# Kernel tuning notes

Measured on AMD Instinct MI355X. Metric: run time of the kernel, lower is better.

The kernel has to match this reference:

```python
import math
import jax, jax.numpy as jnp
import numpy as np

B, L, D = 2, 2048, 1024
NH = 16
HS = D // NH
BLOCK_SIZE = 2048


def setup_inputs() -> dict:
    key = jax.random.key(0)
    ks = jax.random.split(key, 4)
    x = jax.random.normal(ks[0], (B, L, D), dtype=jnp.float32)
    Wqkv = jax.random.normal(ks[1], (D, 3 * D), dtype=jnp.float32) * 0.02
    bqkv = jnp.zeros((3 * D,), dtype=jnp.float32)
    Wproj = jax.random.normal(ks[2], (D, D), dtype=jnp.float32) * 0.02
    bproj = jnp.zeros((D,), dtype=jnp.float32)
    Er = jax.random.normal(ks[3], (BLOCK_SIZE, HS), dtype=jnp.float32)
    return {"x": x, "Wqkv": Wqkv, "bqkv": bqkv, "Wproj": Wproj, "bproj": bproj, "Er": Er}


def _skew(QEr):
    # QEr: [B, nh, L, L]  (Music Transformer skew trick)
    b, nh, nr, nc = QEr.shape
    padded = jnp.pad(QEr, ((0, 0), (0, 0), (0, 0), (1, 0)))  # [B, nh, nr, nc+1]
    reshaped = padded.reshape(b, nh, nc + 1, nr)
    return reshaped[:, :, 1:, :]  # [B, nh, nr, nc]


def reference(x, Wqkv, bqkv, Wproj, bproj, Er):
    b, l, d = x.shape
    qkv = x @ Wqkv + bqkv  # [B, L, 3D]
    q, k, v = jnp.split(qkv, 3, axis=2)
    q = q.reshape(b, l, NH, HS).transpose(0, 2, 1, 3)  # [B, nh, L, hs]
    k = k.reshape(b, l, NH, HS).transpose(0, 2, 1, 3)
    v = v.reshape(b, l, NH, HS).transpose(0, 2, 1, 3)

    start = BLOCK_SIZE - l
    Er_t = Er[start:, :].T  # [hs, L]
    QEr = jnp.einsum('bhld,dm->bhlm', q, Er_t)  # [B, nh, L, L]
    Srel = _skew(QEr)

    QK_t = jnp.einsum('bhld,bhmd->bhlm', q, k)
    scale = 1.0 / math.sqrt(HS)
    att = (QK_t + Srel) * scale
    causal = jnp.tril(jnp.ones((l, l), dtype=bool))
    att = jnp.where(causal[None, None, :, :], att, jnp.float32(-jnp.inf))
    att = jax.nn.softmax(att, axis=-1)
    y = jnp.einsum('bhlm,bhmd->bhld', att, v)
    y = y.transpose(0, 2, 1, 3).reshape(b, l, d)
    return y @ Wproj + bproj
```

## Files before the change

### kernel.cpp

```cpp
#include <hip/hip_runtime.h>
#include <stdint.h>

#define BB 2
#define LL 2048
#define DD 1024
#define NHH 16
#define HSS 64

typedef __bf16 bf16x8 __attribute__((ext_vector_type(8)));
typedef float f32x4 __attribute__((ext_vector_type(4)));

__device__ __forceinline__ bf16x8 load8(const float* p) {
  float4 f0 = *(const float4*)p;
  float4 f1 = *(const float4*)(p + 4);
  bf16x8 v;
  v[0] = (__bf16)f0.x; v[1] = (__bf16)f0.y; v[2] = (__bf16)f0.z; v[3] = (__bf16)f0.w;
  v[4] = (__bf16)f1.x; v[5] = (__bf16)f1.y; v[6] = (__bf16)f1.z; v[7] = (__bf16)f1.w;
  return v;
}
__device__ __forceinline__ bf16x8 load8(const __bf16* p) {
  return *(const bf16x8*)p;
}

__device__ __forceinline__ void async_ld16(__bf16* lds_uniform_base,
                                           const __bf16* gptr_per_lane) {
  __builtin_amdgcn_global_load_lds(
      (const __attribute__((address_space(1))) void*)gptr_per_lane,
      (__attribute__((address_space(3))) void*)lds_uniform_base, 16, 0, 0);
}

__global__ void prep_k(const float* __restrict__ Wqkv, const float* __restrict__ x,
                       const float* __restrict__ Er, __bf16* __restrict__ WqkvT,
                       __bf16* __restrict__ xb, __bf16* __restrict__ Erb) {
  int tx = threadIdx.x, ty = threadIdx.y;
  int tid = ty * 32 + tx;
  if (blockIdx.z == 1) {
    if (blockIdx.x >= 2048) return;
    size_t off = ((size_t)blockIdx.x * 256 + tid) * 8;
    *(bf16x8*)&xb[off] = load8(&x[off]);
    return;
  }
  if (blockIdx.z == 2) {
    if (blockIdx.x >= 64) return;
    size_t off = ((size_t)blockIdx.x * 256 + tid) * 8;
    *(bf16x8*)&Erb[off] = load8(&Er[off]);
    return;
  }
  __shared__ __bf16 tile[32][33];
  int c0 = (blockIdx.x % 96) * 32, r0 = (blockIdx.x / 96) * 32;
#pragma unroll
  for (int i = ty; i < 32; i += 8)
    tile[i][tx] = (__bf16)Wqkv[(size_t)(r0 + i) * 3072 + c0 + tx];
  __syncthreads();
#pragma unroll
  for (int i = ty; i < 32; i += 8)
    WqkvT[(size_t)(c0 + i) * 1024 + r0 + tx] = tile[tx][i];
}

__global__ void tconv_k(const float* __restrict__ src, __bf16* __restrict__ dst,
                        int R, int C) {
  __shared__ __bf16 tile[32][33];
  int c0 = blockIdx.x * 32, r0 = blockIdx.y * 32;
  int tx = threadIdx.x, ty = threadIdx.y;
#pragma unroll
  for (int i = ty; i < 32; i += 8)
    tile[i][tx] = (__bf16)src[(size_t)(r0 + i) * C + c0 + tx];
  __syncthreads();
#pragma unroll
  for (int i = ty; i < 32; i += 8)
    dst[(size_t)(c0 + i) * R + r0 + tx] = tile[tx][i];
}

__global__ __launch_bounds__(256) void gemm_qkv_k(
    const __bf16* __restrict__ A, const __bf16* __restrict__ Bt,
    const float* __restrict__ bias, __bf16* __restrict__ Qo,
    __bf16* __restrict__ Ko, __bf16* __restrict__ Vto) {
  const int K = 1024;
  __shared__ __align__(16) __bf16 As[128 * 32];
  __shared__ __align__(16) __bf16 Bs[128 * 32];
  int t = threadIdx.x;
  int wave = t >> 6, lane = t & 63, qd = lane >> 4, lr = lane & 15;
  int m0 = blockIdx.y * 128, n0 = blockIdx.x * 128;
  int wm = (wave >> 1) * 64, wn = (wave & 1) * 64;
  f32x4 acc[4][4] = {};
  int srow = lane >> 2, sch = (lane & 3) * 8;
  const __bf16* Ab[2];
  const __bf16* Bb[2];
#pragma unroll
  for (int c = 0; c < 2; c++) {
    Ab[c] = A + (size_t)(m0 + (wave * 2 + c) * 16 + srow) * K + sch;
    Bb[c] = Bt + (size_t)(n0 + (wave * 2 + c) * 16 + srow) * K + sch;
  }
  for (int k0 = 0; k0 < K; k0 += 32) {
    __syncthreads();
#pragma unroll
    for (int c = 0; c < 2; c++) {
      async_ld16(&As[(wave * 2 + c) * 512], Ab[c] + k0);
      async_ld16(&Bs[(wave * 2 + c) * 512], Bb[c] + k0);
    }
    __syncthreads();
    bf16x8 af[4], bfr[4];
#pragma unroll
    for (int mt = 0; mt < 4; mt++)
      af[mt] = *(const bf16x8*)&As[(wm + mt * 16 + lr) * 32 + qd * 8];
#pragma unroll
    for (int nt = 0; nt < 4; nt++)
      bfr[nt] = *(const bf16x8*)&Bs[(wn + nt * 16 + lr) * 32 + qd * 8];
#pragma unroll
    for (int mt = 0; mt < 4; mt++)
#pragma unroll
      for (int nt = 0; nt < 4; nt++)
        acc[mt][nt] = __builtin_amdgcn_mfma_f32_16x16x32_bf16(af[mt], bfr[nt],
                                                              acc[mt][nt], 0, 0, 0);
  }
  float bvv[4];
#pragma unroll
  for (int nt = 0; nt < 4; nt++) bvv[nt] = bias[n0 + wn + nt * 16 + lr];
#pragma unroll
  for (int mt = 0; mt < 4; mt++)
#pragma unroll
    for (int nt = 0; nt < 4; nt++)
#pragma unroll
      for (int r = 0; r < 4; r++) {
        int row = m0 + wm + mt * 16 + qd * 4 + r;
        int col = n0 + wn + nt * 16 + lr;
        __bf16 bb = (__bf16)(acc[mt][nt][r] + bvv[nt]);
        int b = row >> 11, l = row & 2047;
        int h = (col >> 6) & 15, d = col & 63;
        if (col < DD) {
          Qo[(((size_t)(b * NHH + h)) * LL + l) * HSS + d] = bb;
        } else if (col < 2 * DD) {
          Ko[(((size_t)(b * NHH + h)) * LL + l) * HSS + d] = bb;
        } else {
          Vto[(((size_t)(b * NHH + h)) * HSS + d) * LL + l] = bb;
        }
      }
}

__global__ __launch_bounds__(256) void gemm_proj_k(
    const __bf16* __restrict__ A, const __bf16* __restrict__ Bt,
    const float* __restrict__ bias, float* __restrict__ out) {
  const int K = 1024, N = 1024;
  __shared__ __align__(16) __bf16 As[128 * 32];
  __shared__ __align__(16) __bf16 Bs[64 * 32];
  int t = threadIdx.x;
  int wave = t >> 6, lane = t & 63, qd = lane >> 4, lr = lane & 15;
  int m0 = blockIdx.y * 128, n0 = blockIdx.x * 64;
  int wm = (wave >> 1) * 64, wn = (wave & 1) * 32;
  f32x4 acc[4][2] = {};
  int srow = lane >> 2, sch = (lane & 3) * 8;
  const __bf16* Ab[2];
  const __bf16* Bb;
#pragma unroll
  for (int c = 0; c < 2; c++)
    Ab[c] = A + (size_t)(m0 + (wave * 2 + c) * 16 + srow) * K + sch;
  Bb = Bt + (size_t)(n0 + wave * 16 + srow) * K + sch;

  for (int k0 = 0; k0 < K; k0 += 32) {
    __syncthreads();
#pragma unroll
    for (int c = 0; c < 2; c++)
      async_ld16(&As[(wave * 2 + c) * 512], Ab[c] + k0);
    async_ld16(&Bs[wave * 512], Bb + k0);
    __syncthreads();
    bf16x8 af[4], bfr[2];
#pragma unroll
    for (int mt = 0; mt < 4; mt++)
      af[mt] = *(const bf16x8*)&As[(wm + mt * 16 + lr) * 32 + qd * 8];
#pragma unroll
    for (int nt = 0; nt < 2; nt++)
      bfr[nt] = *(const bf16x8*)&Bs[(wn + nt * 16 + lr) * 32 + qd * 8];
#pragma unroll
    for (int mt = 0; mt < 4; mt++)
#pragma unroll
      for (int nt = 0; nt < 2; nt++)
        acc[mt][nt] = __builtin_amdgcn_mfma_f32_16x16x32_bf16(af[mt], bfr[nt],
                                                              acc[mt][nt], 0, 0, 0);
  }
  float bvv[2];
#pragma unroll
  for (int nt = 0; nt < 2; nt++) bvv[nt] = bias[n0 + wn + nt * 16 + lr];
#pragma unroll
  for (int mt = 0; mt < 4; mt++)
#pragma unroll
    for (int nt = 0; nt < 2; nt++)
#pragma unroll
      for (int r = 0; r < 4; r++) {
        int row = m0 + wm + mt * 16 + qd * 4 + r;
        int col = n0 + wn + nt * 16 + lr;
        out[(size_t)row * N + col] = acc[mt][nt][r] + bvv[nt];
      }
}

__global__ __launch_bounds__(256, 3) void flash_k(
    const __bf16* __restrict__ Qg, const __bf16* __restrict__ Kg,
    const __bf16* __restrict__ Vtg, const __bf16* __restrict__ Erb,
    __bf16* __restrict__ Po0, __bf16* __restrict__ Po1,
    float* __restrict__ Lp0, float* __restrict__ Lp1) {
  __shared__ __align__(16) __bf16 Kld[64 * 72];
  __shared__ __align__(16) __bf16 Vld[64 * 72];
  __shared__ __align__(16) __bf16 Pball[4][16 * 72];

  int bh = blockIdx.x;
  int tile = 31 - (int)blockIdx.y;
  int i0 = tile * 64;
  int niter = tile + 1;
  int mid = (niter + 1) >> 1;
  int it0 = (blockIdx.z == 0) ? 0 : mid;
  int it1 = (blockIdx.z == 0) ? mid : niter;
  const __bf16* Qh = Qg + (size_t)bh * LL * HSS;
  const __bf16* Kh = Kg + (size_t)bh * LL * HSS;
  const __bf16* Vth = Vtg + (size_t)bh * HSS * LL;
  int b = bh >> 4, h = bh & 15;
  int t = threadIdx.x, wave = t >> 6, lane = t & 63, qd = lane >> 4, lr = lane & 15;
  __bf16* Pb = &Pball[wave][0];
  int cbase = 48 - wave * 16;

  const float SC = 0.18033688011112042f;

  bf16x8 bones;
#pragma unroll
  for (int q = 0; q < 8; q++) bones[q] = (lr == 0) ? (__bf16)1.f : (__bf16)0.f;

  int jj = t >> 2, hf = t & 3;

  int idx4[4], hiv[4], pbv[4], giv[4];
#pragma unroll
  for (int r = 0; r < 4; r++) {
    int tr = qd * 4 + r;
    int base = 15 - tr + lr;
    idx4[r] = (qd * 16 + (base & 15)) << 2;
    hiv[r] = base >> 4;
    pbv[r] = tr * 72 + lr;
    giv[r] = i0 + wave * 16 + tr;
  }

  bf16x8 aq[2];
  {
    const __bf16* qrow = Qh + (size_t)(i0 + wave * 16 + lr) * HSS + qd * 8;
    aq[0] = *(const bf16x8*)qrow;
    aq[1] = *(const bf16x8*)(qrow + 32);
  }
  f32x4 oacc[5] = {};

  bf16x8 kr0, kr1, vr0, vr1;
  auto prefetch = [&](int j0) {
    kr0 = *(const bf16x8*)&Kh[(size_t)(j0 + jj) * HSS + hf * 16];
    kr1 = *(const bf16x8*)&Kh[(size_t)(j0 + jj) * HSS + hf * 16 + 8];
    vr0 = *(const bf16x8*)&Vth[(size_t)jj * LL + j0 + hf * 16];
    vr1 = *(const bf16x8*)&Vth[(size_t)jj * LL + j0 + hf * 16 + 8];
  };
  if (it0 < it1) prefetch(it0 * 64);

  for (int it = it0; it < it1; ++it) {
    int j0 = it * 64;
    __syncthreads();
    *(bf16x8*)&Kld[jj * 72 + hf * 16] = kr0;
    *(bf16x8*)&Kld[jj * 72 + hf * 16 + 8] = kr1;
    *(bf16x8*)&Vld[jj * 72 + hf * 16] = vr0;
    *(bf16x8*)&Vld[jj * 72 + hf * 16 + 8] = vr1;
    __syncthreads();
    if (it + 1 < it1) prefetch((it + 1) * 64);

    int ebase = LL - 64 - i0 + j0 + cbase + lr;
    int e[5];
#pragma unroll
    for (int ct = 0; ct < 5; ct++) {
      int v = ebase + ct * 16;
      e[ct] = (v < LL) ? v : (LL - 1);
    }
    bf16x8 ef0[5];
#pragma unroll
    for (int ct = 0; ct < 5; ct++)
      ef0[ct] = *(const bf16x8*)&Erb[(size_t)e[ct] * HSS + qd * 8];

    f32x4 sacc[4] = {};
    __builtin_amdgcn_s_setprio(1);
#pragma unroll
    for (int ct = 0; ct < 4; ct++)
#pragma unroll
      for (int kc = 0; kc < 2; kc++) {
        bf16x8 bk = *(const bf16x8*)&Kld[(ct * 16 + lr) * 72 + kc * 32 + qd * 8];
        sacc[ct] = __builtin_amdgcn_mfma_f32_16x16x32_bf16(aq[kc], bk, sacc[ct], 0, 0, 0);
      }
    __builtin_amdgcn_s_setprio(0);

    bf16x8 ef1[5];
#pragma unroll
    for (int ct = 0; ct < 5; ct++)
      ef1[ct] = *(const bf16x8*)&Erb[(size_t)e[ct] * HSS + 32 + qd * 8];

    f32x4 racc[5] = {};
    __builtin_amdgcn_s_setprio(1);
#pragma unroll
    for (int ct = 0; ct < 5; ct++)
      racc[ct] = __builtin_amdgcn_mfma_f32_16x16x32_bf16(aq[0], ef0[ct], racc[ct], 0, 0, 0);
#pragma unroll
    for (int ct = 0; ct < 5; ct++)
      racc[ct] = __builtin_amdgcn_mfma_f32_16x16x32_bf16(aq[1], ef1[ct], racc[ct], 0, 0, 0);
    __builtin_amdgcn_s_setprio(0);

#pragma unroll
    for (int r = 0; r < 4; r++) {
      float sh[5];
#pragma unroll
      for (int ct = 0; ct < 5; ct++)
        sh[ct] = __int_as_float(
            __builtin_amdgcn_ds_bpermute(idx4[r], __float_as_int(racc[ct][r])));
      int di = giv[r] - j0;
#pragma unroll
      for (int ct2 = 0; ct2 < 4; ct2++) {
        float rel = hiv[r] ? sh[ct2 + 1] : sh[ct2];
        float p = __builtin_exp2f((sacc[ct2][r] + rel) * SC);
        p = (ct2 * 16 + lr <= di) ? p : 0.f;
        Pb[pbv[r] + ct2 * 16] = (__bf16)p;
      }
    }

    bf16x8 ap0 = *(const bf16x8*)&Pb[lr * 72 + qd * 8];
    bf16x8 ap1 = *(const bf16x8*)&Pb[lr * 72 + 32 + qd * 8];
    __builtin_amdgcn_s_setprio(1);
#pragma unroll
    for (int dt = 0; dt < 4; dt++) {
      bf16x8 bv0 = *(const bf16x8*)&Vld[(dt * 16 + lr) * 72 + qd * 8];
      bf16x8 bv1 = *(const bf16x8*)&Vld[(dt * 16 + lr) * 72 + 32 + qd * 8];
      oacc[dt] = __builtin_amdgcn_mfma_f32_16x16x32_bf16(ap0, bv0, oacc[dt], 0, 0, 0);
      oacc[dt] = __builtin_amdgcn_mfma_f32_16x16x32_bf16(ap1, bv1, oacc[dt], 0, 0, 0);
    }
    oacc[4] = __builtin_amdgcn_mfma_f32_16x16x32_bf16(ap0, bones, oacc[4], 0, 0, 0);
    oacc[4] = __builtin_amdgcn_mfma_f32_16x16x32_bf16(ap1, bones, oacc[4], 0, 0, 0);
    __builtin_amdgcn_s_setprio(0);
  }

  __bf16* Po = (blockIdx.z == 0) ? Po0 : Po1;
  float* Lp = (blockIdx.z == 0) ? Lp0 : Lp1;
#pragma unroll
  for (int r = 0; r < 4; r++) {
    int l = i0 + wave * 16 + qd * 4 + r;
    if (lr == 0) Lp[(size_t)bh * LL + l] = oacc[4][r];
#pragma unroll
    for (int dt = 0; dt < 4; dt++) {
      int d = dt * 16 + lr;
      Po[((size_t)(b * LL) + l) * DD + h * HSS + d] = (__bf16)oacc[dt][r];
    }
  }
}

__global__ void combine_k(const __bf16* __restrict__ Po0,
                          const __bf16* __restrict__ Po1,
                          const float* __restrict__ Lp0,
                          const float* __restrict__ Lp1,
                          __bf16* __restrict__ Y) {
  size_t f = ((size_t)blockIdx.x * 256 + threadIdx.x) * 8;
  int dfull = (int)(f & 1023);
  int h = dfull >> 6;
  int l = (int)((f >> 10) & 2047);
  int b = (int)(f >> 21);
  size_t lidx = ((size_t)(b * NHH + h)) * LL + l;
  float linv = 1.f / (Lp0[lidx] + Lp1[lidx]);
  bf16x8 a = *(const bf16x8*)&Po0[f];
  bf16x8 c = *(const bf16x8*)&Po1[f];
  bf16x8 o;
#pragma unroll
  for (int q = 0; q < 8; q++)
    o[q] = (__bf16)(((float)a[q] + (float)c[q]) * linv);
  *(bf16x8*)&Y[f] = o;
}

extern "C" void kernel_launch(void* const* d_in, const int* in_sizes, int n_in,
                              void* d_out, int out_size, void* d_ws, size_t ws_size,
                              hipStream_t stream) {
  const float* x = (const float*)d_in[0];
  const float* Wqkv = (const float*)d_in[1];
  const float* bqkv = (const float*)d_in[2];
  const float* Wproj = (const float*)d_in[3];
  const float* bproj = (const float*)d_in[4];
  const float* Er = (const float*)d_in[5];
  float* out = (float*)d_out;

  if (ws_size < 4u * 8388608u) return;

  uint8_t* w = (uint8_t*)d_ws;
  __bf16* Q = (__bf16*)w;  w += (size_t)BB * NHH * LL * HSS * 2;
  __bf16* Kt = (__bf16*)w; w += (size_t)BB * NHH * LL * HSS * 2;
  __bf16* Vt = (__bf16*)w; w += (size_t)BB * NHH * LL * HSS * 2;
  __bf16* Y = (__bf16*)w;  w += (size_t)BB * LL * DD * 2;

  __bf16* WqkvT = (__bf16*)d_out;
  __bf16* xb = (__bf16*)((uint8_t*)d_out + (size_t)3072 * 1024 * 2);
  __bf16* Erb = (__bf16*)((uint8_t*)d_out + (size_t)3072 * 1024 * 2 + (size_t)4096 * 1024 * 2);
  __bf16* Po1 = (__bf16*)d_out;
  float* Lp0 = (float*)((uint8_t*)d_out + (size_t)BB * LL * DD * 2);
  float* Lp1 = (float*)((uint8_t*)d_out + (size_t)BB * LL * DD * 2 + (size_t)BB * NHH * LL * 4);
  __bf16* Po0 = Y;
  __bf16* WprojT = Q;

  prep_k<<<dim3(3072, 1, 3), dim3(32, 8), 0, stream>>>(Wqkv, x, Er, WqkvT, xb, Erb);
  gemm_qkv_k<<<dim3(3072 / 128, 4096 / 128), 256, 0, stream>>>(
      xb, WqkvT, bqkv, Q, Kt, Vt);
  flash_k<<<dim3(BB * NHH, 32, 2), 256, 0, stream>>>(
      Q, Kt, Vt, Erb, Po0, Po1, Lp0, Lp1);
  combine_k<<<dim3(2048), 256, 0, stream>>>(Po0, Po1, Lp0, Lp1, Y);
  tconv_k<<<dim3(1024 / 32, 1024 / 32), dim3(32, 8), 0, stream>>>(Wproj, WprojT, 1024, 1024);
  gemm_proj_k<<<dim3(1024 / 64, 4096 / 128), 256, 0, stream>>>(Y, WprojT, bproj, out);
}
```

Measured before the change: 248.1 us.

## Load K and V MFMA operands directly from global memory, dropping LDS staging

The flash attention kernel no longer stages K and V tiles through shared memory with register prefetch and two block barriers per iteration. Each wave now reads its MFMA B-operands for K and V straight from global memory, relying on L1/L2 caching to serve the four waves that read the same data. This removes the barriers and LDS traffic but adds redundant global loads per wave and exposes their latency, since nothing is prefetched ahead.

```diff
diff --git a/kernel.cpp b/kernel.cpp
--- a/kernel.cpp
+++ b/kernel.cpp
@@ -197,8 +197,6 @@
     const __bf16* __restrict__ Vtg, const __bf16* __restrict__ Erb,
     __bf16* __restrict__ Po0, __bf16* __restrict__ Po1,
     float* __restrict__ Lp0, float* __restrict__ Lp1) {
-  __shared__ __align__(16) __bf16 Kld[64 * 72];
-  __shared__ __align__(16) __bf16 Vld[64 * 72];
   __shared__ __align__(16) __bf16 Pball[4][16 * 72];
 
   int bh = blockIdx.x;
@@ -222,8 +220,6 @@
 #pragma unroll
   for (int q = 0; q < 8; q++) bones[q] = (lr == 0) ? (__bf16)1.f : (__bf16)0.f;
 
-  int jj = t >> 2, hf = t & 3;
-
   int idx4[4], hiv[4], pbv[4], giv[4];
 #pragma unroll
   for (int r = 0; r < 4; r++) {
@@ -243,24 +239,11 @@
   }
   f32x4 oacc[5] = {};
 
-  bf16x8 kr0, kr1, vr0, vr1;
-  auto prefetch = [&](int j0) {
-    kr0 = *(const bf16x8*)&Kh[(size_t)(j0 + jj) * HSS + hf * 16];
-    kr1 = *(const bf16x8*)&Kh[(size_t)(j0 + jj) * HSS + hf * 16 + 8];
-    vr0 = *(const bf16x8*)&Vth[(size_t)jj * LL + j0 + hf * 16];
-    vr1 = *(const bf16x8*)&Vth[(size_t)jj * LL + j0 + hf * 16 + 8];
-  };
-  if (it0 < it1) prefetch(it0 * 64);
+  const __bf16* Kln = Kh + (size_t)lr * HSS + qd * 8;
+  const __bf16* Vln = Vth + (size_t)lr * LL + qd * 8;
 
   for (int it = it0; it < it1; ++it) {
     int j0 = it * 64;
-    __syncthreads();
-    *(bf16x8*)&Kld[jj * 72 + hf * 16] = kr0;
-    *(bf16x8*)&Kld[jj * 72 + hf * 16 + 8] = kr1;
-    *(bf16x8*)&Vld[jj * 72 + hf * 16] = vr0;
-    *(bf16x8*)&Vld[jj * 72 + hf * 16 + 8] = vr1;
-    __syncthreads();
-    if (it + 1 < it1) prefetch((it + 1) * 64);
 
     int ebase = LL - 64 - i0 + j0 + cbase + lr;
     int e[5];
@@ -275,14 +258,15 @@
       ef0[ct] = *(const bf16x8*)&Erb[(size_t)e[ct] * HSS + qd * 8];
 
     f32x4 sacc[4] = {};
+    const __bf16* Kit = Kln + (size_t)j0 * HSS;
     __builtin_amdgcn_s_setprio(1);
 #pragma unroll
-    for (int ct = 0; ct < 4; ct++)
-#pragma unroll
-      for (int kc = 0; kc < 2; kc++) {
-        bf16x8 bk = *(const bf16x8*)&Kld[(ct * 16 + lr) * 72 + kc * 32 + qd * 8];
-        sacc[ct] = __builtin_amdgcn_mfma_f32_16x16x32_bf16(aq[kc], bk, sacc[ct], 0, 0, 0);
-      }
+    for (int ct = 0; ct < 4; ct++) {
+      bf16x8 bk0 = *(const bf16x8*)&Kit[(size_t)(ct * 16) * HSS];
+      bf16x8 bk1 = *(const bf16x8*)&Kit[(size_t)(ct * 16) * HSS + 32];
+      sacc[ct] = __builtin_amdgcn_mfma_f32_16x16x32_bf16(aq[0], bk0, sacc[ct], 0, 0, 0);
+      sacc[ct] = __builtin_amdgcn_mfma_f32_16x16x32_bf16(aq[1], bk1, sacc[ct], 0, 0, 0);
+    }
     __builtin_amdgcn_s_setprio(0);
 
     bf16x8 ef1[5];
@@ -319,11 +303,12 @@
 
     bf16x8 ap0 = *(const bf16x8*)&Pb[lr * 72 + qd * 8];
     bf16x8 ap1 = *(const bf16x8*)&Pb[lr * 72 + 32 + qd * 8];
+    const __bf16* Vit = Vln + j0;
     __builtin_amdgcn_s_setprio(1);
 #pragma unroll
     for (int dt = 0; dt < 4; dt++) {
-      bf16x8 bv0 = *(const bf16x8*)&Vld[(dt * 16 + lr) * 72 + qd * 8];
-      bf16x8 bv1 = *(const bf16x8*)&Vld[(dt * 16 + lr) * 72 + 32 + qd * 8];
+      bf16x8 bv0 = *(const bf16x8*)&Vit[(size_t)(dt * 16) * LL];
+      bf16x8 bv1 = *(const bf16x8*)&Vit[(size_t)(dt * 16) * LL + 32];
       oacc[dt] = __builtin_amdgcn_mfma_f32_16x16x32_bf16(ap0, bv0, oacc[dt], 0, 0, 0);
       oacc[dt] = __builtin_amdgcn_mfma_f32_16x16x32_bf16(ap1, bv1, oacc[dt], 0, 0, 0);
     }
```

Result: slower. 361.3 us (+45.6%).

## Pair complementary causal tiles per block and compute row sums in registers

Applied to the files above, without the earlier changes.

Each flash block now handles two query tiles (y and 31-y), so every block does the same 33 key iterations, split evenly at 17 between the two z halves. This balances work across blocks under the causal mask and halves the grid. The extra MFMA that multiplied P by a ones vector to get row sums is replaced by accumulating the bf16-rounded probabilities in registers plus a shuffle reduction. The Er loads are also issued before the barrier so their latency overlaps the LDS stores. The risk is less parallelism, with 1024 blocks instead of 2048, and a longer serial loop per block.

```diff
diff --git a/kernel.cpp b/kernel.cpp
--- a/kernel.cpp
+++ b/kernel.cpp
@@ -202,12 +202,13 @@
   __shared__ __align__(16) __bf16 Pball[4][16 * 72];
 
   int bh = blockIdx.x;
-  int tile = 31 - (int)blockIdx.y;
-  int i0 = tile * 64;
-  int niter = tile + 1;
-  int mid = (niter + 1) >> 1;
-  int it0 = (blockIdx.z == 0) ? 0 : mid;
-  int it1 = (blockIdx.z == 0) ? mid : niter;
+  int y = blockIdx.y;
+  int z = blockIdx.z;
+  int tiles0 = 31 - y;
+  int tiles1 = y;
+  int nA = tiles0 + 1;
+  int cs = z ? 17 : 0, ce = z ? 33 : 17;
+
   const __bf16* Qh = Qg + (size_t)bh * LL * HSS;
   const __bf16* Kh = Kg + (size_t)bh * LL * HSS;
   const __bf16* Vth = Vtg + (size_t)bh * HSS * LL;
@@ -218,13 +219,9 @@
 
   const float SC = 0.18033688011112042f;
 
-  bf16x8 bones;
-#pragma unroll
-  for (int q = 0; q < 8; q++) bones[q] = (lr == 0) ? (__bf16)1.f : (__bf16)0.f;
-
   int jj = t >> 2, hf = t & 3;
 
-  int idx4[4], hiv[4], pbv[4], giv[4];
+  int idx4[4], hiv[4], pbv[4];
 #pragma unroll
   for (int r = 0; r < 4; r++) {
     int tr = qd * 4 + r;
@@ -232,116 +229,140 @@
     idx4[r] = (qd * 16 + (base & 15)) << 2;
     hiv[r] = base >> 4;
     pbv[r] = tr * 72 + lr;
-    giv[r] = i0 + wave * 16 + tr;
-  }
-
-  bf16x8 aq[2];
-  {
-    const __bf16* qrow = Qh + (size_t)(i0 + wave * 16 + lr) * HSS + qd * 8;
-    aq[0] = *(const bf16x8*)qrow;
-    aq[1] = *(const bf16x8*)(qrow + 32);
-  }
-  f32x4 oacc[5] = {};
+  }
+
+  __bf16* Po = (z == 0) ? Po0 : Po1;
+  float* Lp = (z == 0) ? Lp0 : Lp1;
 
   bf16x8 kr0, kr1, vr0, vr1;
-  auto prefetch = [&](int j0) {
-    kr0 = *(const bf16x8*)&Kh[(size_t)(j0 + jj) * HSS + hf * 16];
-    kr1 = *(const bf16x8*)&Kh[(size_t)(j0 + jj) * HSS + hf * 16 + 8];
-    vr0 = *(const bf16x8*)&Vth[(size_t)jj * LL + j0 + hf * 16];
-    vr1 = *(const bf16x8*)&Vth[(size_t)jj * LL + j0 + hf * 16 + 8];
-  };
-  if (it0 < it1) prefetch(it0 * 64);
-
-  for (int it = it0; it < it1; ++it) {
-    int j0 = it * 64;
-    __syncthreads();
-    *(bf16x8*)&Kld[jj * 72 + hf * 16] = kr0;
-    *(bf16x8*)&Kld[jj * 72 + hf * 16 + 8] = kr1;
-    *(bf16x8*)&Vld[jj * 72 + hf * 16] = vr0;
-    *(bf16x8*)&Vld[jj * 72 + hf * 16 + 8] = vr1;
-    __syncthreads();
-    if (it + 1 < it1) prefetch((it + 1) * 64);
-
-    int ebase = LL - 64 - i0 + j0 + cbase + lr;
-    int e[5];
-#pragma unroll
-    for (int ct = 0; ct < 5; ct++) {
-      int v = ebase + ct * 16;
-      e[ct] = (v < LL) ? v : (LL - 1);
+
+#pragma unroll 1
+  for (int ph = 0; ph < 2; ph++) {
+    int tile = ph ? tiles1 : tiles0;
+    int base = ph ? nA : 0;
+    int ni = tile + 1;
+    int it0 = min(max(cs - base, 0), ni);
+    int it1 = min(max(ce - base, 0), ni);
+    int i0 = tile * 64;
+
+    int giv[4];
+#pragma unroll
+    for (int r = 0; r < 4; r++) giv[r] = i0 + wave * 16 + qd * 4 + r;
+
+    bf16x8 aq[2];
+    {
+      const __bf16* qrow = Qh + (size_t)(i0 + wave * 16 + lr) * HSS + qd * 8;
+      aq[0] = *(const bf16x8*)qrow;
+      aq[1] = *(const bf16x8*)(qrow + 32);
     }
-    bf16x8 ef0[5];
-#pragma unroll
-    for (int ct = 0; ct < 5; ct++)
-      ef0[ct] = *(const bf16x8*)&Erb[(size_t)e[ct] * HSS + qd * 8];
-
-    f32x4 sacc[4] = {};
-    __builtin_amdgcn_s_setprio(1);
-#pragma unroll
-    for (int ct = 0; ct < 4; ct++)
-#pragma unroll
-      for (int kc = 0; kc < 2; kc++) {
-        bf16x8 bk = *(const bf16x8*)&Kld[(ct * 16 + lr) * 72 + kc * 32 + qd * 8];
-        sacc[ct] = __builtin_amdgcn_mfma_f32_16x16x32_bf16(aq[kc], bk, sacc[ct], 0, 0, 0);
-      }
-    __builtin_amdgcn_s_setprio(0);
-
-    bf16x8 ef1[5];
-#pragma unroll
-    for (int ct = 0; ct < 5; ct++)
-      ef1[ct] = *(const bf16x8*)&Erb[(size_t)e[ct] * HSS + 32 + qd * 8];
-
-    f32x4 racc[5] = {};
-    __builtin_amdgcn_s_setprio(1);
-#pragma unroll
-    for (int ct = 0; ct < 5; ct++)
-      racc[ct] = __builtin_amdgcn_mfma_f32_16x16x32_bf16(aq[0], ef0[ct], racc[ct], 0, 0, 0);
-#pragma unroll
-    for (int ct = 0; ct < 5; ct++)
-      racc[ct] = __builtin_amdgcn_mfma_f32_16x16x32_bf16(aq[1], ef1[ct], racc[ct], 0, 0, 0);
-    __builtin_amdgcn_s_setprio(0);
+    f32x4 oacc[4] = {};
+    float lsum[4] = {};
+
+    auto prefetch = [&](int j0) {
+      kr0 = *(const bf16x8*)&Kh[(size_t)(j0 + jj) * HSS + hf * 16];
+      kr1 = *(const bf16x8*)&Kh[(size_t)(j0 + jj) * HSS + hf * 16 + 8];
+      vr0 = *(const bf16x8*)&Vth[(size_t)jj * LL + j0 + hf * 16];
+      vr1 = *(const bf16x8*)&Vth[(size_t)jj * LL + j0 + hf * 16 + 8];
+    };
+    if (it0 < it1) prefetch(it0 * 64);
+
+    for (int it = it0; it < it1; ++it) {
+      int j0 = it * 64;
+
+      int ebase = LL - 64 - i0 + j0 + cbase + lr;
+      int e[5];
+#pragma unroll
+      for (int ct = 0; ct < 5; ct++) {
+        int v = ebase + ct * 16;
+        e[ct] = (v < LL) ? v : (LL - 1);
+      }
+      bf16x8 ef0[5];
+#pragma unroll
+      for (int ct = 0; ct < 5; ct++)
+        ef0[ct] = *(const bf16x8*)&Erb[(size_t)e[ct] * HSS + qd * 8];
+
+      __syncthreads();
+      *(bf16x8*)&Kld[jj * 72 + hf * 16] = kr0;
+      *(bf16x8*)&Kld[jj * 72 + hf * 16 + 8] = kr1;
+      *(bf16x8*)&Vld[jj * 72 + hf * 16] = vr0;
+      *(bf16x8*)&Vld[jj * 72 + hf * 16 + 8] = vr1;
+      __syncthreads();
+      if (it + 1 < it1) prefetch((it + 1) * 64);
+
+      f32x4 sacc[4] = {};
+      __builtin_amdgcn_s_setprio(1);
+#pragma unroll
+      for (int ct = 0; ct < 4; ct++)
+#pragma unroll
+        for (int kc = 0; kc < 2; kc++) {
+          bf16x8 bk = *(const bf16x8*)&Kld[(ct * 16 + lr) * 72 + kc * 32 + qd * 8];
+          sacc[ct] = __builtin_amdgcn_mfma_f32_16x16x32_bf16(aq[kc], bk, sacc[ct], 0, 0, 0);
+        }
+      __builtin_amdgcn_s_setprio(0);
+
+      bf16x8 ef1[5];
+#pragma unroll
+      for (int ct = 0; ct < 5; ct++)
+        ef1[ct] = *(const bf16x8*)&Erb[(size_t)e[ct] * HSS + 32 + qd * 8];
+
+      f32x4 racc[5] = {};
+      __builtin_amdgcn_s_setprio(1);
+#pragma unroll
+      for (int ct = 0; ct < 5; ct++)
+        racc[ct] = __builtin_amdgcn_mfma_f32_16x16x32_bf16(aq[0], ef0[ct], racc[ct], 0, 0, 0);
+#pragma unroll
+      for (int ct = 0; ct < 5; ct++)
+        racc[ct] = __builtin_amdgcn_mfma_f32_16x16x32_bf16(aq[1], ef1[ct], racc[ct], 0, 0, 0);
+      __builtin_amdgcn_s_setprio(0);
+
+#pragma unroll
+      for (int r = 0; r < 4; r++) {
+        float sh[5];
+#pragma unroll
+        for (int ct = 0; ct < 5; ct++)
+          sh[ct] = __int_as_float(
+              __builtin_amdgcn_ds_bpermute(idx4[r], __float_as_int(racc[ct][r])));
+        int di = giv[r] - j0;
+#pragma unroll
+        for (int ct2 = 0; ct2 < 4; ct2++) {
+          float rel = hiv[r] ? sh[ct2 + 1] : sh[ct2];
+          float p = __builtin_exp2f((sacc[ct2][r] + rel) * SC);
+          p = (ct2 * 16 + lr <= di) ? p : 0.f;
+          __bf16 pb = (__bf16)p;
+          lsum[r] += (float)pb;
+          Pb[pbv[r] + ct2 * 16] = pb;
+        }
+      }
+
+      bf16x8 ap0 = *(const bf16x8*)&Pb[lr * 72 + qd * 8];
+      bf16x8 ap1 = *(const bf16x8*)&Pb[lr * 72 + 32 + qd * 8];
+      __builtin_amdgcn_s_setprio(1);
+#pragma unroll
+      for (int dt = 0; dt < 4; dt++) {
+        bf16x8 bv0 = *(const bf16x8*)&Vld[(dt * 16 + lr) * 72 + qd * 8];
+        bf16x8 bv1 = *(const bf16x8*)&Vld[(dt * 16 + lr) * 72 + 32 + qd * 8];
+        oacc[dt] = __builtin_amdgcn_mfma_f32_16x16x32_bf16(ap0, bv0, oacc[dt], 0, 0, 0);
+        oacc[dt] = __builtin_amdgcn_mfma_f32_16x16x32_bf16(ap1, bv1, oacc[dt], 0, 0, 0);
+      }
+      __builtin_amdgcn_s_setprio(0);
+    }
 
 #pragma unroll
     for (int r = 0; r < 4; r++) {
-      float sh[5];
-#pragma unroll
-      for (int ct = 0; ct < 5; ct++)
-        sh[ct] = __int_as_float(
-            __builtin_amdgcn_ds_bpermute(idx4[r], __float_as_int(racc[ct][r])));
-      int di = giv[r] - j0;
-#pragma unroll
-      for (int ct2 = 0; ct2 < 4; ct2++) {
-        float rel = hiv[r] ? sh[ct2 + 1] : sh[ct2];
-        float p = __builtin_exp2f((sacc[ct2][r] + rel) * SC);
-        p = (ct2 * 16 + lr <= di) ? p : 0.f;
-        Pb[pbv[r] + ct2 * 16] = (__bf16)p;
-      }
+#pragma unroll
+      for (int m = 1; m < 16; m <<= 1)
+        lsum[r] += __shfl_xor(lsum[r], m, 64);
     }
 
-    bf16x8 ap0 = *(const bf16x8*)&Pb[lr * 72 + qd * 8];
-    bf16x8 ap1 = *(const bf16x8*)&Pb[lr * 72 + 32 + qd * 8];
-    __builtin_amdgcn_s_setprio(1);
-#pragma unroll
-    for (int dt = 0; dt < 4; dt++) {
-      bf16x8 bv0 = *(const bf16x8*)&Vld[(dt * 16 + lr) * 72 + qd * 8];
-      bf16x8 bv1 = *(const bf16x8*)&Vld[(dt * 16 + lr) * 72 + 32 + qd * 8];
-      oacc[dt] = __builtin_amdgcn_mfma_f32_16x16x32_bf16(ap0, bv0, oacc[dt], 0, 0, 0);
-      oacc[dt] = __builtin_amdgcn_mfma_f32_16x16x32_bf16(ap1, bv1, oacc[dt], 0, 0, 0);
-    }
-    oacc[4] = __builtin_amdgcn_mfma_f32_16x16x32_bf16(ap0, bones, oacc[4], 0, 0, 0);
-    oacc[4] = __builtin_amdgcn_mfma_f32_16x16x32_bf16(ap1, bones, oacc[4], 0, 0, 0);
-    __builtin_amdgcn_s_setprio(0);
-  }
-
-  __bf16* Po = (blockIdx.z == 0) ? Po0 : Po1;
-  float* Lp = (blockIdx.z == 0) ? Lp0 : Lp1;
-#pragma unroll
-  for (int r = 0; r < 4; r++) {
-    int l = i0 + wave * 16 + qd * 4 + r;
-    if (lr == 0) Lp[(size_t)bh * LL + l] = oacc[4][r];
-#pragma unroll
-    for (int dt = 0; dt < 4; dt++) {
-      int d = dt * 16 + lr;
-      Po[((size_t)(b * LL) + l) * DD + h * HSS + d] = (__bf16)oacc[dt][r];
+#pragma unroll
+    for (int r = 0; r < 4; r++) {
+      int l = i0 + wave * 16 + qd * 4 + r;
+      if (lr == 0) Lp[(size_t)bh * LL + l] = lsum[r];
+#pragma unroll
+      for (int dt = 0; dt < 4; dt++) {
+        int d = dt * 16 + lr;
+        Po[((size_t)(b * LL) + l) * DD + h * HSS + d] = (__bf16)oacc[dt][r];
+      }
     }
   }
 }
@@ -398,7 +419,7 @@
   prep_k<<<dim3(3072, 1, 3), dim3(32, 8), 0, stream>>>(Wqkv, x, Er, WqkvT, xb, Erb);
   gemm_qkv_k<<<dim3(3072 / 128, 4096 / 128), 256, 0, stream>>>(
       xb, WqkvT, bqkv, Q, Kt, Vt);
-  flash_k<<<dim3(BB * NHH, 32, 2), 256, 0, stream>>>(
+  flash_k<<<dim3(BB * NHH, 16, 2), 256, 0, stream>>>(
       Q, Kt, Vt, Erb, Po0, Po1, Lp0, Lp1);
   combine_k<<<dim3(2048), 256, 0, stream>>>(Po0, Po1, Lp0, Lp1, Y);
   tconv_k<<<dim3(1024 / 32, 1024 / 32), dim3(32, 8), 0, stream>>>(Wproj, WprojT, 1024, 1024);
```

New measurement: 260.9 us. +5.2%, slower.
